# Performance work log

Hardware: AMD Instinct MI355X
Metric: run time of the kernel (lower is better)

Reference implementation:

```python
import jax, jax.numpy as jnp
import numpy as np

VOCAB = 32000
EMBED = 256
UNITS = 1024
BATCH = 16
SEQ = 128


def setup_inputs() -> dict:
    key = jax.random.key(0)
    ks = jax.random.split(key, 7)
    scale_in = 1.0 / np.sqrt(EMBED + UNITS)
    return {
        "inputs": jax.random.randint(ks[0], (BATCH, SEQ), 0, VOCAB, dtype=jnp.int64),
        "emb": jax.random.normal(ks[1], (VOCAB, EMBED), dtype=jnp.float32) * 0.05,
        "W": jax.random.normal(ks[2], (EMBED, 4 * UNITS), dtype=jnp.float32) * scale_in,
        "U": jax.random.normal(ks[3], (UNITS, 4 * UNITS), dtype=jnp.float32) * scale_in,
        "b": jnp.zeros((4 * UNITS,), dtype=jnp.float32),
        "Wc": jax.random.normal(ks[5], (UNITS, VOCAB), dtype=jnp.float32) * (1.0 / np.sqrt(UNITS)),
        "bc": jnp.zeros((VOCAB,), dtype=jnp.float32),
    }


def reference(inputs, emb, W, U, b, Wc, bc):
    # Embedding lookup: [B, T] -> [B, T, E]
    x = emb[inputs]
    B, T, E = x.shape
    H = U.shape[0]

    def step(carry, xt):
        h, c = carry
        # fused gate pre-activations: [B, 4H]
        z = xt @ W + h @ U + b
        i, f, g, o = jnp.split(z, 4, axis=-1)
        c_new = jax.nn.sigmoid(f) * c + jax.nn.sigmoid(i) * jnp.tanh(g)
        h_new = jax.nn.sigmoid(o) * jnp.tanh(c_new)
        return (h_new, c_new), h_new

    h0 = jnp.zeros((B, H), dtype=x.dtype)
    c0 = jnp.zeros((B, H), dtype=x.dtype)
    (h, c), hs = jax.lax.scan(step, (h0, c0), jnp.swapaxes(x, 0, 1))  # hs: [T, B, H]

    out = jnp.swapaxes(hs, 0, 1).reshape(-1, H)  # [B*T, H]
    logits = out @ Wc + bc                        # [B*T, vocab]
    return logits
```

## Files before the change

### kernel.cpp

```cpp
#include <hip/hip_runtime.h>
#include <hip/hip_bf16.h>
#include <math.h>


#define VOCAB 32000
#define EMBED 256
#define UNITS 1024
#define GATES 4096
#define BATCH 16
#define SEQ 128
#define NB 64

using s16x8 = __attribute__((ext_vector_type(8))) short;
using f16x8 = __attribute__((ext_vector_type(8))) _Float16;
using f32x4 = __attribute__((ext_vector_type(4))) float;

__device__ __forceinline__ unsigned short f16_bits(float x) {
    _Float16 h = (_Float16)x;
    return __builtin_bit_cast(unsigned short, h);
}
__device__ __forceinline__ float f16_f32(unsigned short b) {
    return (float)__builtin_bit_cast(_Float16, b);
}
__device__ __forceinline__ int swz_e(int r, int k) {
    return (r * 64 + k) ^ ((((r & 7) ^ ((r >> 2) & 7))) << 3);
}
__device__ __forceinline__ unsigned long long ld_u64(const unsigned long long* p) {
    return __hip_atomic_load(p, __ATOMIC_RELAXED, __HIP_MEMORY_SCOPE_AGENT);
}
__device__ __forceinline__ unsigned poison_u64(unsigned long long v) {
    return (unsigned)((unsigned)v == 0xFFFFFFFFu) |
           (unsigned)((unsigned)(v >> 32) == 0xFFFFFFFFu);
}

__global__ void __launch_bounds__(256) k_prep(
    const float* __restrict__ U,
    unsigned short* __restrict__ ub_hi,
    unsigned short* __restrict__ ub_lo,
    const int* __restrict__ inputs,
    const float* __restrict__ emb,
    const float* __restrict__ W,
    const float* __restrict__ bias,
    float* __restrict__ xWb) {
    __shared__ __align__(16) char smem_raw[65536];
    const int tid = threadIdx.x;

    if (blockIdx.x < 256) {
        float* lds_u = (float*)smem_raw;
        const int ct = blockIdx.x;
        for (int k = tid; k < 1024; k += 256) {
            const float4* src = (const float4*)(U + (size_t)k * GATES + ct * 16);
            float4* dst = (float4*)(&lds_u[k * 16]);
            dst[0] = src[0]; dst[1] = src[1]; dst[2] = src[2]; dst[3] = src[3];
        }
        __syncthreads();
        const int lane = tid & 63;
        const int coll = lane & 15;
        const int kg = lane >> 4;
        for (int kt = (tid >> 6); kt < 32; kt += 4) {
            const int ks = kt * 32 + kg * 8;
            unsigned short h8[8], l8[8];
#pragma unroll
            for (int e = 0; e < 8; ++e) {
                float v = lds_u[(ks + e) * 16 + coll];
                unsigned short hb = f16_bits(v);
                h8[e] = hb;
                l8[e] = f16_bits(v - f16_f32(hb));
            }
            size_t o = (((size_t)ct * 32 + kt) * 64 + lane) * 8;
            *(s16x8*)(ub_hi + o) = *(const s16x8*)h8;
            *(s16x8*)(ub_lo + o) = *(const s16x8*)l8;
        }
        return;
    }

    const int eb = blockIdx.x - 256;
    const int t   = eb >> 4;
    const int col = (eb & 15) * 256 + tid;
    float (*xs)[EMBED] = (float (*)[EMBED])smem_raw;
    int* toks = (int*)(smem_raw + 16384);
    if (tid < BATCH)
        toks[tid] = inputs[tid * SEQ + t];
    __syncthreads();
    for (int r = 0; r < BATCH; ++r)
        xs[r][tid] = emb[(size_t)toks[r] * EMBED + tid];
    __syncthreads();
    float acc[BATCH];
#pragma unroll
    for (int r = 0; r < BATCH; ++r) acc[r] = 0.f;
    for (int k0 = 0; k0 < EMBED; k0 += 4) {
        float4 xv[BATCH];
#pragma unroll
        for (int r = 0; r < BATCH; ++r)
            xv[r] = *(const float4*)(&xs[r][k0]);
#pragma unroll
        for (int e = 0; e < 4; ++e) {
            float w = W[(size_t)(k0 + e) * GATES + col];
#pragma unroll
            for (int r = 0; r < BATCH; ++r)
                acc[r] += ((const float*)&xv[r])[e] * w;
        }
    }
    const float bb = bias[col];
#pragma unroll
    for (int r = 0; r < BATCH; ++r)
        xWb[((size_t)t * BATCH + r) * GATES + col] = acc[r] + bb;
}

__global__ void __launch_bounds__(512, 2) k_fused(
    const unsigned short* __restrict__ ub_hi,
    const unsigned short* __restrict__ ub_lo,
    const float* __restrict__ xWb,
    unsigned short* __restrict__ hsl,
    const float* __restrict__ Wc,
    const float* __restrict__ bc,
    float* __restrict__ out) {
    __shared__ __align__(16) char smem_raw[32768];
    const int tid  = threadIdx.x;
    const int lane = tid & 63;
    const int w    = tid >> 6;

    if (blockIdx.x < NB) {
        __builtin_amdgcn_s_setprio(1);
        float (*zpart)[4][256] = (float (*)[4][256])smem_raw;
        const int bid = blockIdx.x;
        const int j0  = bid * 16;

        const int b_own  = (tid >> 4) & 15;
        const int jj_own = tid & 15;
        const int j_own  = j0 + jj_own;
        const int hb_e = ((j_own >> 5) * 512) + (((j_own >> 3) & 3) * 16 + b_own) * 8 + (j_own & 7);
        float c_own = 0.f;

        f16x8 Uh[4][4], Ul[4][4];
#pragma unroll
        for (int g = 0; g < 4; ++g)
#pragma unroll
            for (int q = 0; q < 4; ++q) {
                size_t o = (((size_t)(g * 64 + bid) * 32) + (w * 4 + q)) * 512 + lane * 8;
                Uh[g][q] = *(const f16x8*)(ub_hi + o);
                Ul[g][q] = *(const f16x8*)(ub_lo + o);
            }

        for (int t = 0; t < SEQ; ++t) {
            float xw0 = 0.f, xw1 = 0.f, xw2 = 0.f, xw3 = 0.f;
            if (tid < 256) {
                const float* xwp = xWb + ((size_t)t * BATCH + b_own) * GATES + j_own;
                xw0 = xwp[0]; xw1 = xwp[UNITS]; xw2 = xwp[2 * UNITS]; xw3 = xwp[3 * UNITS];
            }

            const unsigned long long* p64 =
                (const unsigned long long*)(hsl + (size_t)t * 32768);

            union HU { unsigned long long q2[2]; f16x8 v; };
            HU hh[4];
            while (true) {
                unsigned bad = 0;
#pragma unroll
                for (int q = 0; q < 4; ++q) {
                    const size_t u = (size_t)(w * 4 + q) * 128 + lane * 2;
                    hh[q].q2[0] = ld_u64(p64 + u);
                    hh[q].q2[1] = ld_u64(p64 + u + 1);
                }
#pragma unroll
                for (int q = 0; q < 4; ++q)
                    bad |= poison_u64(hh[q].q2[0]) | poison_u64(hh[q].q2[1]);
                if (__all((int)(bad == 0))) break;
                __builtin_amdgcn_s_sleep(2);
            }

            f32x4 a0[4], a1[4];
#pragma unroll
            for (int g = 0; g < 4; ++g) {
                a0[g] = (f32x4){0.f, 0.f, 0.f, 0.f};
                a1[g] = (f32x4){0.f, 0.f, 0.f, 0.f};
            }
#pragma unroll
            for (int q = 0; q < 4; ++q)
#pragma unroll
                for (int g = 0; g < 4; ++g) {
                    a0[g] = __builtin_amdgcn_mfma_f32_16x16x32_f16(hh[q].v, Uh[g][q], a0[g], 0, 0, 0);
                    a1[g] = __builtin_amdgcn_mfma_f32_16x16x32_f16(hh[q].v, Ul[g][q], a1[g], 0, 0, 0);
                }

#pragma unroll
            for (int g = 0; g < 4; ++g)
#pragma unroll
                for (int r = 0; r < 4; ++r)
                    zpart[w][g][((lane >> 4) * 4 + r) * 16 + (lane & 15)] =
                        a0[g][r] + a1[g][r];
            __syncthreads();

            if (tid < 256) {
                const int zi_idx = b_own * 16 + jj_own;
                float zi = xw0, zf = xw1, zg = xw2, zo = xw3;
#pragma unroll
                for (int ww = 0; ww < 8; ++ww) {
                    zi += zpart[ww][0][zi_idx];
                    zf += zpart[ww][1][zi_idx];
                    zg += zpart[ww][2][zi_idx];
                    zo += zpart[ww][3][zi_idx];
                }
                float si = 1.f / (1.f + expf(-zi));
                float sf = 1.f / (1.f + expf(-zf));
                float so = 1.f / (1.f + expf(-zo));
                float c_new = sf * c_own + si * tanhf(zg);
                float h_new = so * tanhf(c_new);
                c_own = c_new;

                int hhi = (int)f16_bits(h_new);
                int hhi_nb = __shfl_xor(hhi, 1);
                unsigned short* nh = hsl + (size_t)(t + 1) * 32768;
                if ((tid & 1) == 0) {
                    unsigned hp = (unsigned)(unsigned short)hhi | ((unsigned)(unsigned short)hhi_nb << 16);
                    __hip_atomic_store((unsigned*)(nh + hb_e), hp,
                                       __ATOMIC_RELAXED, __HIP_MEMORY_SCOPE_AGENT);
                }
            }
        }
        return;
    }

    unsigned short* Bs = (unsigned short*)smem_raw;
    const int bidp = blockIdx.x - NB;
    const int mt2 = bidp / 250;
    const int nt  = bidp % 250;
    const int n0 = nt * 128;

    {
        const unsigned long long* gp =
            (const unsigned long long*)(hsl + (size_t)(mt2 * 8 + 8) * 32768);
        {
            const unsigned long long* sp = gp + (size_t)tid * 8;
            unsigned long long v = ld_u64(sp);
            while (poison_u64(v)) {
                __builtin_amdgcn_s_sleep(32);
                v = ld_u64(sp);
            }
        }
        while (true) {
            unsigned bad = 0;
#pragma unroll
            for (int i = 0; i < 8; ++i)
                bad |= poison_u64(ld_u64(gp + (size_t)i * 512 + tid));
            if (__syncthreads_and((int)(bad == 0))) break;
            __builtin_amdgcn_s_sleep(16);
        }
        asm volatile("" ::: "memory");
    }

    const int b_kb  = (tid >> 5) * 8;
    const int b_nb4 = (tid & 31) * 4;
    const int wmt  = (w >> 2) * 4;
    const int wn   = (w & 3) * 32;
    const int lr   = lane & 15;
    const int kg   = lane >> 4;

    f32x4 acc[4][2];
#pragma unroll
    for (int i = 0; i < 4; ++i)
#pragma unroll
        for (int j = 0; j < 2; ++j) acc[i][j] = (f32x4){0.f, 0.f, 0.f, 0.f};

    const unsigned short* aslot[4];
#pragma unroll
    for (int mi = 0; mi < 4; ++mi)
        aslot[mi] = hsl + (size_t)(mt2 * 8 + wmt + mi + 1) * 32768 + lane * 8;

    f16x8 A0h[4], A1h[4];
#pragma unroll
    for (int mi = 0; mi < 4; ++mi) {
        A0h[mi] = *(const f16x8*)(aslot[mi]);
        A1h[mi] = *(const f16x8*)(aslot[mi] + 512);
    }
    float4 rawB[8];
    if (tid < 256) {
#pragma unroll
        for (int i = 0; i < 8; ++i)
            rawB[i] = *(const float4*)(Wc + (size_t)(b_kb + i) * VOCAB + n0 + b_nb4);
    }

    for (int kt = 0; kt < 16; ++kt) {
        __syncthreads();
        if (tid < 256) {
#pragma unroll
            for (int nn = 0; nn < 4; ++nn) {
                unsigned short h8[8];
#pragma unroll
                for (int i = 0; i < 8; ++i)
                    h8[i] = f16_bits(((const float*)&rawB[i])[nn]);
                int e = swz_e(b_nb4 + nn, b_kb);
                *(s16x8*)(&Bs[e]) = *(const s16x8*)h8;
            }
        }
        __syncthreads();
        if (kt < 15 && tid < 256) {
            const int k0n = (kt + 1) * 64;
#pragma unroll
            for (int i = 0; i < 8; ++i)
                rawB[i] = *(const float4*)(Wc + (size_t)(k0n + b_kb + i) * VOCAB + n0 + b_nb4);
        }
        {
            f16x8 bh[2];
#pragma unroll
            for (int ni = 0; ni < 2; ++ni)
                bh[ni] = *(const f16x8*)(&Bs[swz_e(wn + ni * 16 + lr, kg * 8)]);
#pragma unroll
            for (int mi = 0; mi < 4; ++mi)
#pragma unroll
                for (int ni = 0; ni < 2; ++ni)
                    acc[mi][ni] = __builtin_amdgcn_mfma_f32_16x16x32_f16(A0h[mi], bh[ni], acc[mi][ni], 0, 0, 0);
            if (kt < 15) {
                const int base = (kt + 1) * 1024;
#pragma unroll
                for (int mi = 0; mi < 4; ++mi)
                    A0h[mi] = *(const f16x8*)(aslot[mi] + base);
            }
        }
        {
            f16x8 bh[2];
#pragma unroll
            for (int ni = 0; ni < 2; ++ni)
                bh[ni] = *(const f16x8*)(&Bs[swz_e(wn + ni * 16 + lr, 32 + kg * 8)]);
#pragma unroll
            for (int mi = 0; mi < 4; ++mi)
#pragma unroll
                for (int ni = 0; ni < 2; ++ni)
                    acc[mi][ni] = __builtin_amdgcn_mfma_f32_16x16x32_f16(A1h[mi], bh[ni], acc[mi][ni], 0, 0, 0);
            if (kt < 15) {
                const int base = (kt + 1) * 1024 + 512;
#pragma unroll
                for (int mi = 0; mi < 4; ++mi)
                    A1h[mi] = *(const f16x8*)(aslot[mi] + base);
            }
        }
    }

    float bcv[2];
#pragma unroll
    for (int ni = 0; ni < 2; ++ni) bcv[ni] = bc[n0 + wn + ni * 16 + lr];
#pragma unroll
    for (int mi = 0; mi < 4; ++mi) {
        const int trow = mt2 * 8 + wmt + mi;
#pragma unroll
        for (int ni = 0; ni < 2; ++ni) {
#pragma unroll
            for (int r = 0; r < 4; ++r) {
                int grow = (kg * 4 + r) * 128 + trow;
                int gcol = n0 + wn + ni * 16 + lr;
                __builtin_nontemporal_store(acc[mi][ni][r] + bcv[ni],
                                            &out[(size_t)grow * VOCAB + gcol]);
            }
        }
    }
}

extern "C" void kernel_launch(void* const* d_in, const int* in_sizes, int n_in,
                              void* d_out, int out_size, void* d_ws, size_t ws_size,
                              hipStream_t stream) {
    const int*   inputs = (const int*)d_in[0];
    const float* emb  = (const float*)d_in[1];
    const float* W    = (const float*)d_in[2];
    const float* U    = (const float*)d_in[3];
    const float* bias = (const float*)d_in[4];
    const float* Wc   = (const float*)d_in[5];
    const float* bc   = (const float*)d_in[6];
    float* out = (float*)d_out;

    char* ws = (char*)d_ws;
    float*          xWb   = (float*)(ws + 0);
    unsigned short* ub_hi = (unsigned short*)(ws + 33554432);
    unsigned short* ub_lo = (unsigned short*)(ws + 41943040);
    unsigned short* hsl   = (unsigned short*)(ws + 50331648);

    hipMemsetAsync(hsl, 0, 65536, stream);
    hipMemsetAsync((char*)hsl + 65536, 0xFF, 8454144 - 65536, stream);

    k_prep<<<256 + 2048, 256, 0, stream>>>(U, ub_hi, ub_lo,
                                           inputs, emb, W, bias, xWb);
    k_fused<<<NB + 4000, 512, 0, stream>>>(ub_hi, ub_lo, xWb, hsl, Wc, bc, out);
}
```

Before: 679.0 us.

## Compute input projection xW+b with fp16 MFMA tiled GEMM in prep kernel

Replaces the scalar FP32 per-timestep input projection (2048 blocks, one column per thread) with a 128x128-tiled GEMM on fp16 MFMA over all B*T rows, converting the gathered embedding rows and W to fp16 in swizzled LDS. The aim is to cut the prep kernel's compute and W reload traffic by reusing tiles across 128 rows and using matrix cores. In exchange it adds fp16 rounding of the embeddings and W (single precision, no hi/lo split) and needs a larger shared-memory layout.

```diff
diff --git a/kernel.cpp b/kernel.cpp
--- a/kernel.cpp
+++ b/kernel.cpp
@@ -74,37 +74,101 @@
         return;
     }
 
-    const int eb = blockIdx.x - 256;
-    const int t   = eb >> 4;
-    const int col = (eb & 15) * 256 + tid;
-    float (*xs)[EMBED] = (float (*)[EMBED])smem_raw;
-    int* toks = (int*)(smem_raw + 16384);
-    if (tid < BATCH)
-        toks[tid] = inputs[tid * SEQ + t];
-    __syncthreads();
-    for (int r = 0; r < BATCH; ++r)
-        xs[r][tid] = emb[(size_t)toks[r] * EMBED + tid];
-    __syncthreads();
-    float acc[BATCH];
-#pragma unroll
-    for (int r = 0; r < BATCH; ++r) acc[r] = 0.f;
-    for (int k0 = 0; k0 < EMBED; k0 += 4) {
-        float4 xv[BATCH];
-#pragma unroll
-        for (int r = 0; r < BATCH; ++r)
-            xv[r] = *(const float4*)(&xs[r][k0]);
-#pragma unroll
-        for (int e = 0; e < 4; ++e) {
-            float w = W[(size_t)(k0 + e) * GATES + col];
-#pragma unroll
-            for (int r = 0; r < BATCH; ++r)
-                acc[r] += ((const float*)&xv[r])[e] * w;
-        }
-    }
-    const float bb = bias[col];
-#pragma unroll
-    for (int r = 0; r < BATCH; ++r)
-        xWb[((size_t)t * BATCH + r) * GATES + col] = acc[r] + bb;
+    unsigned short* As = (unsigned short*)smem_raw;
+    unsigned short* Bs = (unsigned short*)(smem_raw + 16384);
+    int* toks = (int*)(smem_raw + 32768);
+    const int bid2 = blockIdx.x - 256;
+    const int mt = bid2 & 15;
+    const int nt = bid2 >> 4;
+    const int n0 = nt * 128;
+
+    const int lane = tid & 63;
+    const int w4   = tid >> 6;
+    const int wm   = (w4 >> 1) * 64;
+    const int wn   = (w4 & 1) * 64;
+    const int lr   = lane & 15;
+    const int kg   = lane >> 4;
+
+    if (tid < 128) {
+        const int m = mt * 128 + tid;
+        toks[tid] = inputs[(m & 15) * SEQ + (m >> 4)];
+    }
+
+    f32x4 acc[4][4];
+#pragma unroll
+    for (int i = 0; i < 4; ++i)
+#pragma unroll
+        for (int j = 0; j < 4; ++j) acc[i][j] = (f32x4){0.f, 0.f, 0.f, 0.f};
+
+    const int a_r = tid >> 1;
+    const int a_c = (tid & 1) * 32;
+    const int b_kb  = (tid >> 5) * 8;
+    const int b_nb4 = (tid & 31) * 4;
+
+    for (int kt = 0; kt < 4; ++kt) {
+        __syncthreads();
+        {
+            const float* src = emb + (size_t)toks[a_r] * EMBED + kt * 64 + a_c;
+            float4 va[8];
+#pragma unroll
+            for (int i = 0; i < 8; ++i) va[i] = *(const float4*)(src + i * 4);
+#pragma unroll
+            for (int i = 0; i < 4; ++i) {
+                unsigned short h8[8];
+#pragma unroll
+                for (int e = 0; e < 8; ++e)
+                    h8[e] = f16_bits(((const float*)&va[2 * i])[e]);
+                *(s16x8*)(&As[swz_e(a_r, a_c + i * 8)]) = *(const s16x8*)h8;
+            }
+        }
+        {
+            float4 rawB[8];
+#pragma unroll
+            for (int i = 0; i < 8; ++i)
+                rawB[i] = *(const float4*)(W + (size_t)(kt * 64 + b_kb + i) * GATES + n0 + b_nb4);
+#pragma unroll
+            for (int nn = 0; nn < 4; ++nn) {
+                unsigned short h8[8];
+#pragma unroll
+                for (int i = 0; i < 8; ++i)
+                    h8[i] = f16_bits(((const float*)&rawB[i])[nn]);
+                *(s16x8*)(&Bs[swz_e(b_nb4 + nn, b_kb)]) = *(const s16x8*)h8;
+            }
+        }
+        __syncthreads();
+#pragma unroll
+        for (int ks = 0; ks < 2; ++ks) {
+            const int kofs = ks * 32 + kg * 8;
+            f16x8 av[4], bv[4];
+#pragma unroll
+            for (int mi = 0; mi < 4; ++mi)
+                av[mi] = *(const f16x8*)(&As[swz_e(wm + mi * 16 + lr, kofs)]);
+#pragma unroll
+            for (int ni = 0; ni < 4; ++ni)
+                bv[ni] = *(const f16x8*)(&Bs[swz_e(wn + ni * 16 + lr, kofs)]);
+#pragma unroll
+            for (int mi = 0; mi < 4; ++mi)
+#pragma unroll
+                for (int ni = 0; ni < 4; ++ni)
+                    acc[mi][ni] = __builtin_amdgcn_mfma_f32_16x16x32_f16(av[mi], bv[ni], acc[mi][ni], 0, 0, 0);
+        }
+    }
+
+    float bcv[4];
+#pragma unroll
+    for (int ni = 0; ni < 4; ++ni) bcv[ni] = bias[n0 + wn + ni * 16 + lr];
+#pragma unroll
+    for (int mi = 0; mi < 4; ++mi) {
+#pragma unroll
+        for (int ni = 0; ni < 4; ++ni) {
+#pragma unroll
+            for (int r = 0; r < 4; ++r) {
+                int m   = mt * 128 + wm + mi * 16 + kg * 4 + r;
+                int col = n0 + wn + ni * 16 + lr;
+                xWb[(size_t)m * GATES + col] = acc[mi][ni][r] + bcv[ni];
+            }
+        }
+    }
 }
 
 __global__ void __launch_bounds__(512, 2) k_fused(
@@ -376,7 +440,7 @@
     hipMemsetAsync(hsl, 0, 65536, stream);
     hipMemsetAsync((char*)hsl + 65536, 0xFF, 8454144 - 65536, stream);
 
-    k_prep<<<256 + 2048, 256, 0, stream>>>(U, ub_hi, ub_lo,
-                                           inputs, emb, W, bias, xWb);
+    k_prep<<<256 + 512, 256, 0, stream>>>(U, ub_hi, ub_lo,
+                                          inputs, emb, W, bias, xWb);
     k_fused<<<NB + 4000, 512, 0, stream>>>(ub_hi, ub_lo, xWb, hsl, Wc, bc, out);
 }
```

Result: faster. 592.9 us (-12.7%).
